# Kernel optimization log

Hardware: AMD Instinct MI355X
Metric: run time of the kernel (lower is better)

## Reference

```python
import math
import jax, jax.numpy as jnp
import numpy as np

H = 16
D_MODEL = 1024
D_K = D_MODEL // H


def setup_inputs() -> dict:
    key = jax.random.key(0)
    ks = jax.random.split(key, 16)
    B, S = 2, 2048
    s = 1.0 / math.sqrt(D_MODEL)
    inp = {
        "q": jax.random.normal(ks[0], (B, S, D_MODEL), jnp.float32),
        "k": jax.random.normal(ks[1], (B, S, D_MODEL), jnp.float32),
        "v": jax.random.normal(ks[2], (B, S, D_MODEL), jnp.float32),
        "mask": jax.random.randint(ks[3], (B, S), 0, 2, jnp.int32),
        "Wq": jax.random.normal(ks[4], (D_MODEL, D_MODEL), jnp.float32) * s,
        "bq": jnp.zeros((D_MODEL,), jnp.float32),
        "Wk": jax.random.normal(ks[5], (D_MODEL, D_MODEL), jnp.float32) * s,
        "bk": jnp.zeros((D_MODEL,), jnp.float32),
        "Wv": jax.random.normal(ks[6], (D_MODEL, D_MODEL), jnp.float32) * s,
        "bv": jnp.zeros((D_MODEL,), jnp.float32),
        "Wp": jax.random.normal(ks[7], (D_MODEL, D_MODEL), jnp.float32) * s,
        "bp": jnp.zeros((D_MODEL,), jnp.float32),
        "gamma": jnp.ones((D_MODEL,), jnp.float32),
        "beta": jnp.zeros((D_MODEL,), jnp.float32),
    }
    return inp


def reference(q, k, v, mask, Wq, bq, Wk, bk, Wv, bv, Wp, bp, gamma, beta):
    B, S, _ = q.shape
    residual = q
    # projections -> [B, H, S, D_K]
    def split_heads(x):
        return x.reshape(B, S, H, D_K).transpose(0, 2, 1, 3)
    qh = split_heads(q @ Wq + bq)
    kh = split_heads(k @ Wk + bk)
    vh = split_heads(v @ Wv + bv)
    # scores [B, H, S, S]
    scores = jnp.einsum("bhqd,bhkd->bhqk", qh, kh) / math.sqrt(D_K)
    m = mask[:, None, None, :]  # [B,1,1,S_k]
    scores = jnp.where(m == 0, -1e9, scores)
    attn = jax.nn.softmax(scores, axis=-1)  # dropout is identity in eval
    out = jnp.einsum("bhqk,bhkd->bhqd", attn, vh)
    out = out.transpose(0, 2, 1, 3).reshape(B, S, D_MODEL)
    out = out @ Wp + bp
    x = residual + out
    # LayerNorm over last dim, eps=1e-5 (torch default)
    mu = jnp.mean(x, axis=-1, keepdims=True)
    var = jnp.mean((x - mu) ** 2, axis=-1, keepdims=True)
    out = (x - mu) * jax.lax.rsqrt(var + 1e-5) * gamma + beta
    return (out, attn)
```

## Files before the change

kernel.cpp:

```cpp
#include <hip/hip_runtime.h>
#include <hip/hip_bf16.h>

#define HN 16
#define DM 1024
#define DKH 64
#define BB 2
#define SS 2048
#define NT (BB*SS)
#define BK 32

using bf16   = __bf16;
using bf16x4 = __attribute__((ext_vector_type(4))) __bf16;
using bf16x8 = __attribute__((ext_vector_type(8))) __bf16;
using f32x4  = __attribute__((ext_vector_type(4))) float;

__device__ __forceinline__ void gload16(bf16* lds, const bf16* g) {
    __builtin_amdgcn_global_load_lds(
        (const __attribute__((address_space(1))) unsigned int*)g,
        (__attribute__((address_space(3))) unsigned int*)lds, 16, 0, 0);
}

__global__ __launch_bounds__(256) void convert_qkv(
    const float* __restrict__ q, const float* __restrict__ k,
    const float* __restrict__ v, bf16* __restrict__ dst)
{
    const int z = blockIdx.z;
    const float* src = (z == 0) ? q : (z == 1) ? k : v;
    bf16* d = dst + (size_t)z * NT * DM;
    int i = blockIdx.x * 256 + threadIdx.x;
    const int n4 = NT * DM / 4;
    if (i < n4) {
        float4 f = ((const float4*)src)[i];
        bf16x4 o = { (bf16)f.x, (bf16)f.y, (bf16)f.z, (bf16)f.w };
        ((bf16x4*)d)[i] = o;
    }
}

__global__ __launch_bounds__(256) void transpose_w(
    const float* __restrict__ Wq, const float* __restrict__ Wk,
    const float* __restrict__ Wv, const float* __restrict__ Wp,
    bf16* __restrict__ dst)
{
    const int z = blockIdx.z;
    const float* W = (z == 0) ? Wq : (z == 1) ? Wk : (z == 2) ? Wv : Wp;
    bf16* WT = dst + (size_t)z * DM * DM;
    __shared__ float t[64][65];
    const int tx = threadIdx.x;
    const int r0 = blockIdx.y * 64, c0 = blockIdx.x * 64;
    {
        const int row = tx >> 2, cb = (tx & 3) * 16;
        const float4* src = (const float4*)(W + (size_t)(r0 + row) * DM + c0 + cb);
        #pragma unroll
        for (int i = 0; i < 4; i++) {
            float4 f = src[i];
            t[row][cb + i*4 + 0] = f.x; t[row][cb + i*4 + 1] = f.y;
            t[row][cb + i*4 + 2] = f.z; t[row][cb + i*4 + 3] = f.w;
        }
    }
    __syncthreads();
    {
        const int n = tx >> 2, kb = (tx & 3) * 16;
        bf16 buf[16];
        #pragma unroll
        for (int i = 0; i < 16; i++) buf[i] = (bf16)t[kb + i][n];
        bf16* outp = WT + (size_t)(c0 + n) * DM + r0 + kb;
        *(bf16x8*)(outp)     = *(bf16x8*)(&buf[0]);
        *(bf16x8*)(outp + 8) = *(bf16x8*)(&buf[8]);
    }
}

__device__ __forceinline__ void gemm_core_128(
    const bf16* __restrict__ A, const bf16* __restrict__ Bt,
    int row0, int col0, bf16* As, bf16* Bs, f32x4 (&acc)[4][4])
{
    const int t = threadIdx.x;
    const int lane = t & 63, w = t >> 6;
    const int wr = w >> 1, wc = w & 1;
    const int lg = lane >> 4, l16 = lane & 15;
    const int srow = lane >> 2, scol = (lane & 3) * 8;
    const bf16* gA0 = A  + (size_t)(row0 + w*32 +      srow) * DM + scol;
    const bf16* gA1 = A  + (size_t)(row0 + w*32 + 16 + srow) * DM + scol;
    const bf16* gB0 = Bt + (size_t)(col0 + w*32 +      srow) * DM + scol;
    const bf16* gB1 = Bt + (size_t)(col0 + w*32 + 16 + srow) * DM + scol;
    bf16* lA0 = As + (w*32     ) * BK;
    bf16* lA1 = As + (w*32 + 16) * BK;
    bf16* lB0 = Bs + (w*32     ) * BK;
    bf16* lB1 = Bs + (w*32 + 16) * BK;

    for (int k0 = 0; k0 < DM; k0 += BK) {
        gload16(lA0, gA0 + k0);
        gload16(lA1, gA1 + k0);
        gload16(lB0, gB0 + k0);
        gload16(lB1, gB1 + k0);
        __syncthreads();
        bf16x8 af[4], bfr[4];
        #pragma unroll
        for (int m = 0; m < 4; m++)
            af[m] = *(const bf16x8*)(As + (wr*64 + m*16 + l16) * BK + lg*8);
        #pragma unroll
        for (int n = 0; n < 4; n++)
            bfr[n] = *(const bf16x8*)(Bs + (wc*64 + n*16 + l16) * BK + lg*8);
        #pragma unroll
        for (int m = 0; m < 4; m++)
            #pragma unroll
            for (int n = 0; n < 4; n++)
                acc[m][n] = __builtin_amdgcn_mfma_f32_16x16x32_bf16(af[m], bfr[n], acc[m][n], 0, 0, 0);
        __syncthreads();
    }
}

__global__ __launch_bounds__(256) void gemm_qkv(
    const bf16* __restrict__ qkvb, const bf16* __restrict__ wT,
    const float* __restrict__ bq, const float* __restrict__ bk,
    const float* __restrict__ bv, bf16* __restrict__ outbase)
{
    __shared__ __align__(16) bf16 As[128 * BK];
    __shared__ __align__(16) bf16 Bs[128 * BK];
    const int z = blockIdx.z;
    const bf16* A;
    const bf16* Bt;
    int row0, col0;
    if (z != 2) {
        A    = qkvb + (size_t)z * NT * DM;
        Bt   = wT   + (size_t)z * DM * DM;
        row0 = blockIdx.y * 128;
        col0 = blockIdx.x * 128;
    } else {
        A    = wT   + (size_t)2 * DM * DM;
        Bt   = qkvb + (size_t)2 * NT * DM;
        row0 = blockIdx.x * 128;
        col0 = blockIdx.y * 128;
    }

    f32x4 acc[4][4] = {};
    gemm_core_128(A, Bt, row0, col0, As, Bs, acc);

    const int t = threadIdx.x, lane = t & 63, w = t >> 6;
    const int wr = w >> 1, wc = w & 1, lg = lane >> 4, l16 = lane & 15;

    if (z == 0) {
        bf16* outp = outbase;
        const float qscale = 0.125f * 1.44269504f;
        #pragma unroll
        for (int m = 0; m < 4; m++) {
            #pragma unroll
            for (int n = 0; n < 4; n++) {
                const int col = col0 + wc*64 + n*16 + l16;
                const float bcol = bq[col];
                const int h = col >> 6, dk = col & 63;
                #pragma unroll
                for (int r = 0; r < 4; r++) {
                    const int row = row0 + wr*64 + m*16 + lg*4 + r;
                    const int b = row >> 11, s = row & (SS - 1);
                    const float val = (acc[m][n][r] + bcol) * qscale;
                    outp[(((size_t)b*HN + h)*SS + s)*DKH + dk] = (bf16)val;
                }
            }
        }
    } else if (z == 1) {
        bf16* outp = outbase + (size_t)NT * DM;
        #pragma unroll
        for (int m = 0; m < 4; m++) {
            #pragma unroll
            for (int n = 0; n < 4; n++) {
                const int col = col0 + wc*64 + n*16 + l16;
                const float bcol = bk[col];
                const int h = col >> 6, d = col & 63;
                #pragma unroll
                for (int r = 0; r < 4; r++) {
                    const int row = row0 + wr*64 + m*16 + lg*4 + r;
                    const int b = row >> 11, s = row & (SS - 1);
                    const float val = acc[m][n][r] + bcol;
                    const size_t bh = (size_t)b*HN + h;
                    const size_t idx = bh*SS*DKH
                        + (size_t)(((s>>4)*2 + (d>>5))*512)
                        + ((s&15)*4 + ((d>>3)&3))*8 + (d&7);
                    outp[idx] = (bf16)val;
                }
            }
        }
    } else {
        bf16* outp = outbase + (size_t)2 * NT * DM;
        #pragma unroll
        for (int m = 0; m < 4; m++) {
            #pragma unroll
            for (int n = 0; n < 4; n++) {
                const int tok = col0 + wc*64 + n*16 + l16;
                const int b = tok >> 11, s = tok & (SS - 1);
                #pragma unroll
                for (int r = 0; r < 4; r++) {
                    const int hdk = row0 + wr*64 + m*16 + lg*4 + r;
                    const int h = hdk >> 6, dk = hdk & 63;
                    const float val = acc[m][n][r] + bv[hdk];
                    const size_t bh = (size_t)b*HN + h;
                    const size_t idx = bh*SS*DKH
                        + (size_t)(((s>>5)*4 + (dk>>4))*512)
                        + ((dk&15)*4 + ((s>>3)&3))*8 + (s&7);
                    outp[idx] = (bf16)val;
                }
            }
        }
    }
}

__global__ __launch_bounds__(256) void attn_kernel(
    const bf16* __restrict__ Qh, const bf16* __restrict__ Kswz,
    const bf16* __restrict__ Vswz, const int* __restrict__ mask,
    float* __restrict__ attn, bf16* __restrict__ Ob)
{
    __shared__ float bias_s[SS];
    __shared__ __align__(16) float pbuf[4][2][16*36];
    const int hwid = blockIdx.x;
    const int vid  = (hwid & 7) * 64 + (hwid >> 3);
    const int bh = vid >> 4;
    const int b  = bh >> 4;
    const int q0 = (vid & 15) * 128;
    const bf16* Kb = Kswz + (size_t)bh * SS * DKH;
    const bf16* Vb = Vswz + (size_t)bh * SS * DKH;
    const bf16* Q  = Qh   + (size_t)bh * SS * DKH;
    const int t = threadIdx.x, w = t >> 6, lane = t & 63;
    const int lg = lane >> 4, l16 = lane & 15;
    const int lp = (l16 << 2) | lg;

    for (int i = t; i < SS; i += 256)
        bias_s[i] = mask[b * SS + i] ? 0.0f : -1.44269504e9f;

    bf16x8 qf[2][2];
    #pragma unroll
    for (int tl = 0; tl < 2; tl++) {
        const bf16* qp = Q + (size_t)(q0 + w*32 + tl*16 + l16)*DKH + lg*8;
        qf[tl][0] = *(const bf16x8*)(qp);
        qf[tl][1] = *(const bf16x8*)(qp + 32);
    }
    __syncthreads();

    float l_[2] = {0.f, 0.f};
    bf16x8 kc0 = *(const bf16x8*)(Kb + lp*8);
    bf16x8 kc1 = *(const bf16x8*)(Kb + 512 + lp*8);
    for (int c = 0; c < 128; c++) {
        const int cn = (c + 1 < 128) ? c + 1 : 127;
        bf16x8 kn0 = *(const bf16x8*)(Kb + (size_t)(cn*2    )*512 + lp*8);
        bf16x8 kn1 = *(const bf16x8*)(Kb + (size_t)(cn*2 + 1)*512 + lp*8);
        const float4 b4 = *(const float4*)(&bias_s[c*16 + lg*4]);
        #pragma unroll
        for (int tl = 0; tl < 2; tl++) {
            f32x4 st = {0.f, 0.f, 0.f, 0.f};
            st = __builtin_amdgcn_mfma_f32_16x16x32_bf16(kc0, qf[tl][0], st, 0, 0, 0);
            st = __builtin_amdgcn_mfma_f32_16x16x32_bf16(kc1, qf[tl][1], st, 0, 0, 0);
            l_[tl] += exp2f(st[0] + b4.x) + exp2f(st[1] + b4.y)
                    + exp2f(st[2] + b4.z) + exp2f(st[3] + b4.w);
        }
        kc0 = kn0; kc1 = kn1;
    }
    float inv_l[2];
    #pragma unroll
    for (int tl = 0; tl < 2; tl++) {
        float l = l_[tl];
        l += __shfl_xor(l, 16);
        l += __shfl_xor(l, 32);
        inv_l[tl] = 1.0f / l;
    }

    float* attn_base = attn + ((size_t)bh * SS + q0 + w*32) * SS;
    f32x4 oacc[2][4] = {};

    bf16x8 ck[4], cv[4];
    #pragma unroll
    for (int h = 0; h < 4; h++) ck[h] = *(const bf16x8*)(Kb + (size_t)h*512 + lp*8);
    #pragma unroll
    for (int n = 0; n < 4; n++) cv[n] = *(const bf16x8*)(Vb + (size_t)n*512 + lp*8);

    for (int j = 0; j < 64; j++) {
        bf16x8 nk[4], nv[4];
        const bool have = (j + 1) < 64;
        if (have) {
            #pragma unroll
            for (int h = 0; h < 4; h++)
                nk[h] = *(const bf16x8*)(Kb + (size_t)((j+1)*4 + h)*512 + lp*8);
            #pragma unroll
            for (int n = 0; n < 4; n++)
                nv[n] = *(const bf16x8*)(Vb + (size_t)((j+1)*4 + n)*512 + lp*8);
        }
        const float4 b40 = *(const float4*)(&bias_s[(2*j    )*16 + lg*4]);
        const float4 b41 = *(const float4*)(&bias_s[(2*j + 1)*16 + lg*4]);
        #pragma unroll
        for (int tl = 0; tl < 2; tl++) {
            float* pb = &pbuf[w][tl][0];
            f32x4 s0 = {0.f, 0.f, 0.f, 0.f};
            s0 = __builtin_amdgcn_mfma_f32_16x16x32_bf16(ck[0], qf[tl][0], s0, 0, 0, 0);
            s0 = __builtin_amdgcn_mfma_f32_16x16x32_bf16(ck[1], qf[tl][1], s0, 0, 0, 0);
            f32x4 s1 = {0.f, 0.f, 0.f, 0.f};
            s1 = __builtin_amdgcn_mfma_f32_16x16x32_bf16(ck[2], qf[tl][0], s1, 0, 0, 0);
            s1 = __builtin_amdgcn_mfma_f32_16x16x32_bf16(ck[3], qf[tl][1], s1, 0, 0, 0);
            const float il = inv_l[tl];
            f32x4 pn0, pn1;
            pn0[0] = exp2f(s0[0] + b40.x) * il;
            pn0[1] = exp2f(s0[1] + b40.y) * il;
            pn0[2] = exp2f(s0[2] + b40.z) * il;
            pn0[3] = exp2f(s0[3] + b40.w) * il;
            pn1[0] = exp2f(s1[0] + b41.x) * il;
            pn1[1] = exp2f(s1[1] + b41.y) * il;
            pn1[2] = exp2f(s1[2] + b41.z) * il;
            pn1[3] = exp2f(s1[3] + b41.w) * il;
            *(f32x4*)(pb + l16*36 + lg*4)      = pn0;
            *(f32x4*)(pb + l16*36 + 16 + lg*4) = pn1;
            f32x4 ra = *(const f32x4*)(pb + l16*36 + lg*8);
            f32x4 rb = *(const f32x4*)(pb + l16*36 + lg*8 + 4);
            bf16x8 pa;
            pa[0] = (bf16)ra[0]; pa[1] = (bf16)ra[1];
            pa[2] = (bf16)ra[2]; pa[3] = (bf16)ra[3];
            pa[4] = (bf16)rb[0]; pa[5] = (bf16)rb[1];
            pa[6] = (bf16)rb[2]; pa[7] = (bf16)rb[3];
            #pragma unroll
            for (int n = 0; n < 4; n++)
                oacc[tl][n] = __builtin_amdgcn_mfma_f32_16x16x32_bf16(pa, cv[n], oacc[tl][n], 0, 0, 0);
            float* sp = attn_base + (size_t)(tl*16 + l16)*SS + j*32 + lg*8;
            *(f32x4*)(sp)     = ra;
            *(f32x4*)(sp + 4) = rb;
        }
        #pragma unroll
        for (int h = 0; h < 4; h++) ck[h] = nk[h];
        #pragma unroll
        for (int n = 0; n < 4; n++) cv[n] = nv[n];
    }

    const int hh = bh & 15;
    #pragma unroll
    for (int tl = 0; tl < 2; tl++) {
        #pragma unroll
        for (int r = 0; r < 4; r++) {
            const int srow = q0 + w*32 + tl*16 + lg*4 + r;
            #pragma unroll
            for (int n = 0; n < 4; n++) {
                const float val = oacc[tl][n][r];
                Ob[((size_t)b*SS + srow)*DM + hh*DKH + n*16 + l16] = (bf16)val;
            }
        }
    }
}

__global__ __launch_bounds__(256) void gemm_out(
    const bf16* __restrict__ Ob, const bf16* __restrict__ WpT,
    const float* __restrict__ bp, const float* __restrict__ resid,
    float* __restrict__ out)
{
    __shared__ __align__(16) bf16 As[128 * BK];
    __shared__ __align__(16) bf16 Bs[128 * BK];
    const int row0 = blockIdx.y * 128, col0 = blockIdx.x * 128;
    f32x4 acc[4][4] = {};
    gemm_core_128(Ob, WpT, row0, col0, As, Bs, acc);

    const int t = threadIdx.x, lane = t & 63, w = t >> 6;
    const int wr = w >> 1, wc = w & 1, lg = lane >> 4, l16 = lane & 15;
    #pragma unroll
    for (int m = 0; m < 4; m++) {
        #pragma unroll
        for (int n = 0; n < 4; n++) {
            const int col = col0 + wc*64 + n*16 + l16;
            const float bcol = bp[col];
            #pragma unroll
            for (int r = 0; r < 4; r++) {
                const int row = row0 + wr*64 + m*16 + lg*4 + r;
                const size_t idx = (size_t)row * DM + col;
                out[idx] = acc[m][n][r] + bcol + resid[idx];
            }
        }
    }
}

__global__ __launch_bounds__(256) void ln_kernel(
    float* __restrict__ x, const float* __restrict__ gamma,
    const float* __restrict__ beta)
{
    const int row = blockIdx.x, t = threadIdx.x;
    float4 v = ((const float4*)(x + (size_t)row * DM))[t];
    float s  = v.x + v.y + v.z + v.w;
    float s2 = v.x*v.x + v.y*v.y + v.z*v.z + v.w*v.w;
    #pragma unroll
    for (int off = 32; off; off >>= 1) {
        s  += __shfl_xor(s, off);
        s2 += __shfl_xor(s2, off);
    }
    __shared__ float rs_[4], rs2_[4];
    const int w = t >> 6;
    if ((t & 63) == 0) { rs_[w] = s; rs2_[w] = s2; }
    __syncthreads();
    s  = rs_[0] + rs_[1] + rs_[2] + rs_[3];
    s2 = rs2_[0] + rs2_[1] + rs2_[2] + rs2_[3];
    const float mu   = s * (1.0f / DM);
    const float var  = s2 * (1.0f / DM) - mu * mu;
    const float rstd = rsqrtf(var + 1e-5f);
    float4 g  = ((const float4*)gamma)[t];
    float4 bb = ((const float4*)beta)[t];
    float4 o;
    o.x = (v.x - mu) * rstd * g.x + bb.x;
    o.y = (v.y - mu) * rstd * g.y + bb.y;
    o.z = (v.z - mu) * rstd * g.z + bb.z;
    o.w = (v.w - mu) * rstd * g.w + bb.w;
    ((float4*)(x + (size_t)row * DM))[t] = o;
}

extern "C" void kernel_launch(void* const* d_in, const int* in_sizes, int n_in,
                              void* d_out, int out_size, void* d_ws, size_t ws_size,
                              hipStream_t stream)
{
    const float* q     = (const float*)d_in[0];
    const float* k     = (const float*)d_in[1];
    const float* v     = (const float*)d_in[2];
    const int*   mask  = (const int*)  d_in[3];
    const float* Wq    = (const float*)d_in[4];
    const float* bq    = (const float*)d_in[5];
    const float* Wk    = (const float*)d_in[6];
    const float* bk    = (const float*)d_in[7];
    const float* Wv    = (const float*)d_in[8];
    const float* bv    = (const float*)d_in[9];
    const float* Wp    = (const float*)d_in[10];
    const float* bp    = (const float*)d_in[11];
    const float* gamma = (const float*)d_in[12];
    const float* beta  = (const float*)d_in[13];

    float* out  = (float*)d_out;
    float* attn = out + (size_t)NT * DM;

    char* wsb = (char*)d_ws;
    bf16* qb   = (bf16*)wsb;
    bf16* wT   = (bf16*)(wsb + 25165824);
    bf16* Qh   = (bf16*)(wsb + 33554432);
    bf16* Ob   = (bf16*)(wsb + 58720256);
    bf16* Kswz = Qh + (size_t)NT * DM;
    bf16* Vswz = Qh + (size_t)2 * NT * DM;

    convert_qkv<<<dim3(4096, 1, 3), 256, 0, stream>>>(q, k, v, qb);
    transpose_w<<<dim3(16, 16, 4), 256, 0, stream>>>(Wq, Wk, Wv, Wp, wT);
    gemm_qkv   <<<dim3(8, 32, 3),  256, 0, stream>>>(qb, wT, bq, bk, bv, Qh);
    attn_kernel<<<dim3(512, 1),    256, 0, stream>>>(Qh, Kswz, Vswz, mask, attn, Ob);
    gemm_out   <<<dim3(8, 32),     256, 0, stream>>>(Ob, wT + 3*1048576, bp, q, out);
    ln_kernel  <<<4096,            256, 0, stream>>>(out, gamma, beta);
}
```

Measured before the change: 353.0 us.

## Feed softmax probabilities to PV MFMA directly from registers, dropping LDS round-trip

Changes the V swizzled layout so the probability fragments from the QK MFMA output can be used directly as operands of 16x16x16 bf16 MFMAs, eliminating the per-tile LDS write/read transpose (pbuf). Normalization by 1/l is deferred to the epilogue via a shuffle, and attention-probability stores are now two 16-byte writes per lane at strided columns. Removes LDS traffic and waits in the inner loop, but doubles the PV MFMA instruction count (K=16 instead of K=32) and changes global store coalescing of the attn matrix.

New measurement: 353.4 us. No clear change (+0.1%).

```diff
diff --git a/kernel.cpp b/kernel.cpp
--- a/kernel.cpp
+++ b/kernel.cpp
@@ -13,6 +13,8 @@
 using bf16x4 = __attribute__((ext_vector_type(4))) __bf16;
 using bf16x8 = __attribute__((ext_vector_type(8))) __bf16;
 using f32x4  = __attribute__((ext_vector_type(4))) float;
+using s16x4  = __attribute__((ext_vector_type(4))) short;
+using s16x8  = __attribute__((ext_vector_type(8))) short;
 
 __device__ __forceinline__ void gload16(bf16* lds, const bf16* g) {
     __builtin_amdgcn_global_load_lds(
@@ -195,7 +197,8 @@
                     const size_t bh = (size_t)b*HN + h;
                     const size_t idx = bh*SS*DKH
                         + (size_t)(((s>>5)*4 + (dk>>4))*512)
-                        + ((dk&15)*4 + ((s>>3)&3))*8 + (s&7);
+                        + (((s>>2)&3)*16 + (dk&15))*8
+                        + ((s>>4)&1)*4 + (s&3);
                     outp[idx] = (bf16)val;
                 }
             }
@@ -209,7 +212,6 @@
     float* __restrict__ attn, bf16* __restrict__ Ob)
 {
     __shared__ float bias_s[SS];
-    __shared__ __align__(16) float pbuf[4][2][16*36];
     const int hwid = blockIdx.x;
     const int vid  = (hwid & 7) * 64 + (hwid >> 3);
     const int bh = vid >> 4;
@@ -268,7 +270,7 @@
     #pragma unroll
     for (int h = 0; h < 4; h++) ck[h] = *(const bf16x8*)(Kb + (size_t)h*512 + lp*8);
     #pragma unroll
-    for (int n = 0; n < 4; n++) cv[n] = *(const bf16x8*)(Vb + (size_t)n*512 + lp*8);
+    for (int n = 0; n < 4; n++) cv[n] = *(const bf16x8*)(Vb + (size_t)n*512 + lane*8);
 
     for (int j = 0; j < 64; j++) {
         bf16x8 nk[4], nv[4];
@@ -279,44 +281,42 @@
                 nk[h] = *(const bf16x8*)(Kb + (size_t)((j+1)*4 + h)*512 + lp*8);
             #pragma unroll
             for (int n = 0; n < 4; n++)
-                nv[n] = *(const bf16x8*)(Vb + (size_t)((j+1)*4 + n)*512 + lp*8);
+                nv[n] = *(const bf16x8*)(Vb + (size_t)((j+1)*4 + n)*512 + lane*8);
         }
         const float4 b40 = *(const float4*)(&bias_s[(2*j    )*16 + lg*4]);
         const float4 b41 = *(const float4*)(&bias_s[(2*j + 1)*16 + lg*4]);
         #pragma unroll
         for (int tl = 0; tl < 2; tl++) {
-            float* pb = &pbuf[w][tl][0];
             f32x4 s0 = {0.f, 0.f, 0.f, 0.f};
             s0 = __builtin_amdgcn_mfma_f32_16x16x32_bf16(ck[0], qf[tl][0], s0, 0, 0, 0);
             s0 = __builtin_amdgcn_mfma_f32_16x16x32_bf16(ck[1], qf[tl][1], s0, 0, 0, 0);
             f32x4 s1 = {0.f, 0.f, 0.f, 0.f};
             s1 = __builtin_amdgcn_mfma_f32_16x16x32_bf16(ck[2], qf[tl][0], s1, 0, 0, 0);
             s1 = __builtin_amdgcn_mfma_f32_16x16x32_bf16(ck[3], qf[tl][1], s1, 0, 0, 0);
+            const float p00 = exp2f(s0[0] + b40.x), p01 = exp2f(s0[1] + b40.y);
+            const float p02 = exp2f(s0[2] + b40.z), p03 = exp2f(s0[3] + b40.w);
+            const float p10 = exp2f(s1[0] + b41.x), p11 = exp2f(s1[1] + b41.y);
+            const float p12 = exp2f(s1[2] + b41.z), p13 = exp2f(s1[3] + b41.w);
+            union { bf16x4 h; s16x4 s; } pk0, pk1;
+            pk0.h = bf16x4{ (bf16)p00, (bf16)p01, (bf16)p02, (bf16)p03 };
+            pk1.h = bf16x4{ (bf16)p10, (bf16)p11, (bf16)p12, (bf16)p13 };
+            #pragma unroll
+            for (int n = 0; n < 4; n++) {
+                union { bf16x8 v; s16x8 s; } vv;
+                vv.v = cv[n];
+                s16x4 vlo = __builtin_shufflevector(vv.s, vv.s, 0, 1, 2, 3);
+                s16x4 vhi = __builtin_shufflevector(vv.s, vv.s, 4, 5, 6, 7);
+                oacc[tl][n] = __builtin_amdgcn_mfma_f32_16x16x16bf16_1k(
+                    pk0.s, vlo, oacc[tl][n], 0, 0, 0);
+                oacc[tl][n] = __builtin_amdgcn_mfma_f32_16x16x16bf16_1k(
+                    pk1.s, vhi, oacc[tl][n], 0, 0, 0);
+            }
             const float il = inv_l[tl];
-            f32x4 pn0, pn1;
-            pn0[0] = exp2f(s0[0] + b40.x) * il;
-            pn0[1] = exp2f(s0[1] + b40.y) * il;
-            pn0[2] = exp2f(s0[2] + b40.z) * il;
-            pn0[3] = exp2f(s0[3] + b40.w) * il;
-            pn1[0] = exp2f(s1[0] + b41.x) * il;
-            pn1[1] = exp2f(s1[1] + b41.y) * il;
-            pn1[2] = exp2f(s1[2] + b41.z) * il;
-            pn1[3] = exp2f(s1[3] + b41.w) * il;
-            *(f32x4*)(pb + l16*36 + lg*4)      = pn0;
-            *(f32x4*)(pb + l16*36 + 16 + lg*4) = pn1;
-            f32x4 ra = *(const f32x4*)(pb + l16*36 + lg*8);
-            f32x4 rb = *(const f32x4*)(pb + l16*36 + lg*8 + 4);
-            bf16x8 pa;
-            pa[0] = (bf16)ra[0]; pa[1] = (bf16)ra[1];
-            pa[2] = (bf16)ra[2]; pa[3] = (bf16)ra[3];
-            pa[4] = (bf16)rb[0]; pa[5] = (bf16)rb[1];
-            pa[6] = (bf16)rb[2]; pa[7] = (bf16)rb[3];
-            #pragma unroll
-            for (int n = 0; n < 4; n++)
-                oacc[tl][n] = __builtin_amdgcn_mfma_f32_16x16x32_bf16(pa, cv[n], oacc[tl][n], 0, 0, 0);
-            float* sp = attn_base + (size_t)(tl*16 + l16)*SS + j*32 + lg*8;
-            *(f32x4*)(sp)     = ra;
-            *(f32x4*)(sp + 4) = rb;
+            f32x4 st0 = { p00*il, p01*il, p02*il, p03*il };
+            f32x4 st1 = { p10*il, p11*il, p12*il, p13*il };
+            float* rowp = attn_base + (size_t)(tl*16 + l16)*SS + j*32 + lg*4;
+            *(f32x4*)(rowp)      = st0;
+            *(f32x4*)(rowp + 16) = st1;
         }
         #pragma unroll
         for (int h = 0; h < 4; h++) ck[h] = nk[h];
@@ -329,10 +329,11 @@
     for (int tl = 0; tl < 2; tl++) {
         #pragma unroll
         for (int r = 0; r < 4; r++) {
+            const float il = __shfl(inv_l[tl], lg*4 + r);
             const int srow = q0 + w*32 + tl*16 + lg*4 + r;
             #pragma unroll
             for (int n = 0; n < 4; n++) {
-                const float val = oacc[tl][n][r];
+                const float val = oacc[tl][n][r] * il;
                 Ob[((size_t)b*SS + srow)*DM + hh*DKH + n*16 + l16] = (bf16)val;
             }
         }
```
